# Optimization experiments

Measured on AMD Instinct MI355X. Metric: run time of the kernel, lower is better.

## Reference

```python
import jax, jax.numpy as jnp
import numpy as np

HEADS = 12
EMBED = 768
HEAD_DIM = EMBED // HEADS


def setup_inputs() -> dict:
    key = jax.random.key(0)
    kx, kw, kb = jax.random.split(key, 3)
    x = jax.random.normal(kx, (8, 1024, EMBED), dtype=jnp.float32)
    # nn.Linear(embed, 3*embed): weight (3E, E), bias (3E,)
    W_qkv = jax.random.normal(kw, (3 * EMBED, EMBED), dtype=jnp.float32) * (1.0 / np.sqrt(EMBED))
    b_qkv = jax.random.normal(kb, (3 * EMBED,), dtype=jnp.float32) * 0.01
    return {"x": x, "W_qkv": W_qkv, "b_qkv": b_qkv}


def reference(x, W_qkv, b_qkv):
    b, n, e = x.shape
    qkv = x @ W_qkv.T + b_qkv                       # (b, n, 3E)
    qkv = qkv.reshape(b, n, HEADS, 3 * HEAD_DIM)    # (b, n, h, 3d)
    q, k, v = jnp.split(qkv, 3, axis=-1)            # each (b, n, h, d)
    scores = jnp.einsum('bihd,bjhd->bijh', q, k) / np.sqrt(HEAD_DIM)
    attn = jax.nn.softmax(scores, axis=-2)          # softmax over keys j (dim=-2)
    out = jnp.einsum('bijh,bjhd->bihd', attn, v)
    return out.reshape(b, n, e)
```

## Files before the change

kernel.cpp:

```cpp
#include <hip/hip_runtime.h>
#include <hip/hip_bf16.h>
#include <cstdint>

#define BATCH 8
#define SEQ   1024
#define EMB   768
#define HEADS 12
#define HDIM  64
#define C3    2304
#define MROWS (BATCH*SEQ)
#define NKT   (EMB / 32)
#define MTILES (MROWS / 128)
#define NTILES (C3 / 128)
#define XPACK_BLOCKS (MTILES * NKT)
#define WPACK_BLOCKS (NTILES * NKT)

typedef __attribute__((ext_vector_type(8)))  short bf16x8;
typedef __attribute__((ext_vector_type(4)))  short bf16x4;
typedef __attribute__((ext_vector_type(4)))  float f32x4;
typedef __attribute__((ext_vector_type(16))) float f32x16;

static __device__ inline short f2bf(float f) {
    union { float f; uint32_t u; } v; v.f = f;
    uint32_t u = v.u + 0x7fff + ((v.u >> 16) & 1);
    return (short)(u >> 16);
}

static __device__ __forceinline__ void gload_lds16(const short* g, short* l) {
    __builtin_amdgcn_global_load_lds(
        (const __attribute__((address_space(1))) unsigned int*)g,
        (__attribute__((address_space(3))) unsigned int*)l, 16, 0, 0);
}

__global__ __launch_bounds__(256) void pack_bf16(const float* __restrict__ x,
                                                 short* __restrict__ xb2,
                                                 const float* __restrict__ W,
                                                 short* __restrict__ Wb2) {
    const float* in;
    short* out;
    int blk;
    if (blockIdx.x < XPACK_BLOCKS) {
        in = x; out = xb2; blk = blockIdx.x;
    } else {
        in = W; out = Wb2; blk = blockIdx.x - XPACK_BLOCKS;
    }
    const int mt = blk / NKT;
    const int kt = blk % NKT;
    short* obase = out + (size_t)blk * 4096;

    #pragma unroll
    for (int p = 0; p < 2; ++p) {
        int idx = p * 256 + threadIdx.x;
        int r = idx >> 2, s = idx & 3;
        const float* src = in + (size_t)(mt * 128 + r) * EMB + kt * 32 + s * 8;
        float4 v0 = ((const float4*)src)[0];
        float4 v1 = ((const float4*)src)[1];
        bf16x8 o = { f2bf(v0.x), f2bf(v0.y), f2bf(v0.z), f2bf(v0.w),
                     f2bf(v1.x), f2bf(v1.y), f2bf(v1.z), f2bf(v1.w) };
        int S = ((4 * r + s) ^ (r & 7));
        *(bf16x8*)(obase + S * 8) = o;
    }
}

__global__ __launch_bounds__(256) void qkv_gemm_mfma(const short* __restrict__ Apk,
                                                     const short* __restrict__ Bpk,
                                                     const float* __restrict__ bias,
                                                     short* __restrict__ qkvb) {
    __shared__ short As[2][4096];
    __shared__ short Bs[2][4096];

    const int g    = blockIdx.x;
    const int xcd  = g & 7;
    const int ring = g >> 3;
    const int by   = xcd * 8 + (ring & 7);
    const int bx   = ring >> 3;

    const int t    = threadIdx.x;
    const int w    = t >> 6;
    const int lane = t & 63;
    const int s4   = lane >> 4;
    const int r15  = lane & 15;
    const int m0 = by * 128, n0 = bx * 128;
    const int wm = (w & 1) * 64, wn = (w >> 1) * 64;

    const short* Ab = Apk + (size_t)by * (NKT * 4096);
    const short* Bb = Bpk + (size_t)bx * (NKT * 4096);

    int offA[4], offB[4];
    #pragma unroll
    for (int i = 0; i < 4; ++i) {
        int ra = wm + i * 16 + r15;
        offA[i] = ((4 * ra + s4) ^ (ra & 7)) << 3;
        int rb = wn + i * 16 + r15;
        offB[i] = ((4 * rb + s4) ^ (rb & 7)) << 3;
    }

    const int seg0 = w * 2;

#define STAGE(buf, kt) do {                                                   \
        const short* _a = Ab + (size_t)(kt) * 4096;                           \
        const short* _b = Bb + (size_t)(kt) * 4096;                           \
        gload_lds16(_a + (seg0    ) * 512 + lane * 8, &As[buf][(seg0    ) * 512]); \
        gload_lds16(_b + (seg0    ) * 512 + lane * 8, &Bs[buf][(seg0    ) * 512]); \
        gload_lds16(_a + (seg0 + 1) * 512 + lane * 8, &As[buf][(seg0 + 1) * 512]); \
        gload_lds16(_b + (seg0 + 1) * 512 + lane * 8, &Bs[buf][(seg0 + 1) * 512]); \
    } while (0)

    f32x4 acc[4][4] = {};

#define COMPUTE(buf) do {                                                     \
        bf16x8 af[4], bff[4];                                                 \
        _Pragma("unroll")                                                     \
        for (int i = 0; i < 4; ++i) {                                         \
            af[i]  = *(const bf16x8*)&As[buf][offA[i]];                       \
            bff[i] = *(const bf16x8*)&Bs[buf][offB[i]];                       \
        }                                                                     \
        _Pragma("unroll")                                                     \
        for (int mi = 0; mi < 4; ++mi)                                        \
            _Pragma("unroll")                                                 \
            for (int ni = 0; ni < 4; ++ni)                                    \
                acc[mi][ni] = __builtin_amdgcn_mfma_f32_16x16x32_bf16(        \
                    af[mi], bff[ni], acc[mi][ni], 0, 0, 0);                   \
    } while (0)

    STAGE(0, 0);
    __syncthreads();

    for (int kt = 0; kt < NKT; kt += 2) {
        STAGE(1, kt + 1);
        COMPUTE(0);
        __syncthreads();
        if (kt + 2 < NKT) STAGE(0, kt + 2);
        COMPUTE(1);
        __syncthreads();
    }
#undef STAGE
#undef COMPUTE

    float bsv[4], scl[4];
    #pragma unroll
    for (int ni = 0; ni < 4; ++ni) {
        int n = n0 + wn + ni * 16 + r15;
        bsv[ni] = bias[n];
        scl[ni] = ((n % 192) < 64) ? 0.125f : 1.0f;
    }
    #pragma unroll
    for (int mi = 0; mi < 4; ++mi)
        #pragma unroll
        for (int ni = 0; ni < 4; ++ni) {
            int n = n0 + wn + ni * 16 + r15;
            #pragma unroll
            for (int reg = 0; reg < 4; ++reg) {
                int m = m0 + wm + mi * 16 + s4 * 4 + reg;
                qkvb[(size_t)m * C3 + n] = f2bf((acc[mi][ni][reg] + bsv[ni]) * scl[ni]);
            }
        }
}

__global__ __launch_bounds__(256) void v_transpose(const short* __restrict__ qkvb,
                                                   short* __restrict__ vt) {
    __shared__ int Lt[64][65];

    const int bh = blockIdx.x;
    const int jt = blockIdx.y;
    const int b = bh / HEADS, h = bh % HEADS;
    const int t = threadIdx.x;
    const int j0 = jt * 64;
    const size_t base = (size_t)b * SEQ * C3 + (size_t)h * 192 + 128;

    #pragma unroll
    for (int p = 0; p < 2; ++p) {
        int idx = p * 256 + t;
        int j = idx >> 3, d0 = (idx & 7) * 8;
        bf16x8 v = *(const bf16x8*)(qkvb + base + (size_t)(j0 + j) * C3 + d0);
        #pragma unroll
        for (int u = 0; u < 8; ++u)
            Lt[d0 + u][j] = (int)(unsigned short)v[u];
    }
    __syncthreads();
    #pragma unroll
    for (int p = 0; p < 2; ++p) {
        int idx = p * 256 + t;
        int d = idx >> 3, c8 = (idx & 7) * 8;
        bf16x8 o;
        #pragma unroll
        for (int u = 0; u < 8; ++u)
            o[u] = (short)Lt[d][c8 + u];
        *(bf16x8*)(vt + ((size_t)bh * 64 + d) * SEQ + j0 + c8) = o;
    }
}

#define LDP 72

__global__ __launch_bounds__(256, 3) void attn_mfma(const short* __restrict__ qkvb,
                                                    const short* __restrict__ vt,
                                                    float* __restrict__ out) {
    __shared__ short Ks[64][LDP];
    __shared__ short Vt[64][LDP];
    __shared__ short Ps[128][LDP];

    const int g    = blockIdx.x;
    const int qt   = g / (BATCH * HEADS);
    const int bh   = g % (BATCH * HEADS);
    const int b    = bh / HEADS;
    const int h    = bh % HEADS;
    const int t    = threadIdx.x;
    const int w    = t >> 6;
    const int lane = t & 63;
    const int c    = lane & 15;
    const int q    = lane >> 4;
    const int i0   = qt * 128;

    const size_t base = (size_t)b * SEQ * C3 + (size_t)h * 192;
    const short* vtb = vt + (size_t)bh * 64 * SEQ;

    #pragma unroll
    for (int p = 0; p < 4; ++p) {
        int idx = p * 256 + t;
        int i = idx >> 3, d0 = (idx & 7) << 3;
        *(bf16x8*)&Ps[i][d0] =
            *(const bf16x8*)(qkvb + base + (size_t)(i0 + i) * C3 + d0);
    }
    __syncthreads();
    bf16x8 aq[2][2];
    #pragma unroll
    for (int s = 0; s < 2; ++s) {
        aq[s][0] = *(bf16x8*)&Ps[w * 32 + s * 16 + c][q * 8];
        aq[s][1] = *(bf16x8*)&Ps[w * 32 + s * 16 + c][32 + q * 8];
    }

    f32x4 o[2][4] = {};
    float l_acc[2] = {0.f, 0.f};

    for (int kt = 0; kt < 16; ++kt) {
        const int j0 = kt * 64;
        __syncthreads();
        #pragma unroll
        for (int p = 0; p < 2; ++p) {
            int idx = p * 256 + t;
            int j = idx >> 3, d0 = (idx & 7) << 3;
            *(bf16x8*)&Ks[j][d0] =
                *(const bf16x8*)(qkvb + base + 64 + (size_t)(j0 + j) * C3 + d0);
        }
        #pragma unroll
        for (int p = 0; p < 2; ++p) {
            int idx = p * 256 + t;
            int d = idx >> 3, j8 = (idx & 7) << 3;
            *(bf16x8*)&Vt[d][j8] =
                *(const bf16x8*)(vtb + (size_t)d * SEQ + j0 + j8);
        }
        __syncthreads();

        bf16x8 ka[4][2];
        #pragma unroll
        for (int mt = 0; mt < 4; ++mt) {
            ka[mt][0] = *(bf16x8*)&Ks[mt * 16 + c][q * 8];
            ka[mt][1] = *(bf16x8*)&Ks[mt * 16 + c][32 + q * 8];
        }

        f32x4 s[2][4];
        #pragma unroll
        for (int ss = 0; ss < 2; ++ss)
            #pragma unroll
            for (int mt = 0; mt < 4; ++mt) {
                f32x4 acc = {0.f, 0.f, 0.f, 0.f};
                acc = __builtin_amdgcn_mfma_f32_16x16x32_bf16(ka[mt][0], aq[ss][0], acc, 0, 0, 0);
                acc = __builtin_amdgcn_mfma_f32_16x16x32_bf16(ka[mt][1], aq[ss][1], acc, 0, 0, 0);
                s[ss][mt] = acc;
            }

        #pragma unroll
        for (int ss = 0; ss < 2; ++ss)
            #pragma unroll
            for (int mt = 0; mt < 4; ++mt) {
                float p0 = __expf(s[ss][mt][0]);
                float p1 = __expf(s[ss][mt][1]);
                float p2 = __expf(s[ss][mt][2]);
                float p3 = __expf(s[ss][mt][3]);
                l_acc[ss] += (p0 + p1) + (p2 + p3);
                bf16x4 pw = { f2bf(p0), f2bf(p1), f2bf(p2), f2bf(p3) };
                *(bf16x4*)&Ps[w * 32 + ss * 16 + c][mt * 16 + 4 * q] = pw;
            }

        bf16x8 vb[4][2];
        #pragma unroll
        for (int dt = 0; dt < 4; ++dt) {
            vb[dt][0] = *(bf16x8*)&Vt[dt * 16 + c][q * 8];
            vb[dt][1] = *(bf16x8*)&Vt[dt * 16 + c][32 + q * 8];
        }

        #pragma unroll
        for (int ss = 0; ss < 2; ++ss) {
            bf16x8 ap0 = *(bf16x8*)&Ps[w * 32 + ss * 16 + c][q * 8];
            bf16x8 ap1 = *(bf16x8*)&Ps[w * 32 + ss * 16 + c][32 + q * 8];
            #pragma unroll
            for (int dt = 0; dt < 4; ++dt) {
                o[ss][dt] = __builtin_amdgcn_mfma_f32_16x16x32_bf16(ap0, vb[dt][0], o[ss][dt], 0, 0, 0);
                o[ss][dt] = __builtin_amdgcn_mfma_f32_16x16x32_bf16(ap1, vb[dt][1], o[ss][dt], 0, 0, 0);
            }
        }
    }

    float linv[2][4];
    #pragma unroll
    for (int ss = 0; ss < 2; ++ss) {
        float v = l_acc[ss];
        v += __shfl_xor(v, 16, 64);
        v += __shfl_xor(v, 32, 64);
        #pragma unroll
        for (int r = 0; r < 4; ++r)
            linv[ss][r] = 1.0f / __shfl(v, 4 * q + r, 64);
    }

    #pragma unroll
    for (int ss = 0; ss < 2; ++ss)
        #pragma unroll
        for (int dt = 0; dt < 4; ++dt)
            #pragma unroll
            for (int r = 0; r < 4; ++r) {
                int i = w * 32 + ss * 16 + q * 4 + r;
                out[((size_t)b * SEQ + i0 + i) * EMB + h * HDIM + dt * 16 + c]
                    = o[ss][dt][r] * linv[ss][r];
            }
}

extern "C" void kernel_launch(void* const* d_in, const int* in_sizes, int n_in,
                              void* d_out, int out_size, void* d_ws, size_t ws_size,
                              hipStream_t stream) {
    const float* x    = (const float*)d_in[0];
    const float* W    = (const float*)d_in[1];
    const float* bias = (const float*)d_in[2];
    float* out = (float*)d_out;

    short* xb2  = (short*)d_ws;
    short* Wb2  = xb2 + (size_t)MROWS * EMB;
    short* qkvb = Wb2 + (size_t)C3 * EMB;
    short* vt   = qkvb + (size_t)MROWS * C3;

    pack_bf16<<<XPACK_BLOCKS + WPACK_BLOCKS, 256, 0, stream>>>(x, xb2, W, Wb2);

    qkv_gemm_mfma<<<1152, 256, 0, stream>>>(xb2, Wb2, bias, qkvb);

    dim3 g2(BATCH * HEADS, SEQ / 64);
    v_transpose<<<g2, 256, 0, stream>>>(qkvb, vt);

    attn_mfma<<<BATCH * HEADS * (SEQ / 128), 256, 0, stream>>>(qkvb, vt, out);
}
```

Baseline: 170.3 us.

## Load K and V fragments directly from global memory, dropping LDS staging

Removes the shared-memory tiles for K and V and the two block barriers per key tile. Each wave now loads its MFMA operand fragments straight from global memory. K for the next tile is prefetched into registers right after the score MFMAs, software-pipelining the loads, and Q is also loaded directly. Each of the four waves now issues its own redundant global/L2 reads of the same K/V tiles instead of sharing one LDS copy. Launch bounds drop from 3 to 2 blocks per SM to leave room for the extra registers.

```diff
diff --git a/kernel.cpp b/kernel.cpp
--- a/kernel.cpp
+++ b/kernel.cpp
@@ -192,11 +192,9 @@
 
 #define LDP 72
 
-__global__ __launch_bounds__(256, 3) void attn_mfma(const short* __restrict__ qkvb,
+__global__ __launch_bounds__(256, 2) void attn_mfma(const short* __restrict__ qkvb,
                                                     const short* __restrict__ vt,
                                                     float* __restrict__ out) {
-    __shared__ short Ks[64][LDP];
-    __shared__ short Vt[64][LDP];
     __shared__ short Ps[128][LDP];
 
     const int g    = blockIdx.x;
@@ -214,48 +212,42 @@
     const size_t base = (size_t)b * SEQ * C3 + (size_t)h * 192;
     const short* vtb = vt + (size_t)bh * 64 * SEQ;
 
-    #pragma unroll
-    for (int p = 0; p < 4; ++p) {
-        int idx = p * 256 + t;
-        int i = idx >> 3, d0 = (idx & 7) << 3;
-        *(bf16x8*)&Ps[i][d0] =
-            *(const bf16x8*)(qkvb + base + (size_t)(i0 + i) * C3 + d0);
-    }
-    __syncthreads();
     bf16x8 aq[2][2];
-    #pragma unroll
-    for (int s = 0; s < 2; ++s) {
-        aq[s][0] = *(bf16x8*)&Ps[w * 32 + s * 16 + c][q * 8];
-        aq[s][1] = *(bf16x8*)&Ps[w * 32 + s * 16 + c][32 + q * 8];
+    {
+        const short* pq = qkvb + base + (size_t)(i0 + w * 32 + c) * C3 + q * 8;
+        #pragma unroll
+        for (int s = 0; s < 2; ++s) {
+            aq[s][0] = *(const bf16x8*)(pq + (size_t)s * 16 * C3);
+            aq[s][1] = *(const bf16x8*)(pq + (size_t)s * 16 * C3 + 32);
+        }
+    }
+
+    const short* pk[4];
+    const short* pv[4];
+    #pragma unroll
+    for (int mt = 0; mt < 4; ++mt)
+        pk[mt] = qkvb + base + 64 + (size_t)(mt * 16 + c) * C3 + q * 8;
+    #pragma unroll
+    for (int dt = 0; dt < 4; ++dt)
+        pv[dt] = vtb + (size_t)(dt * 16 + c) * SEQ + q * 8;
+
+    bf16x8 ka[4][2];
+    #pragma unroll
+    for (int mt = 0; mt < 4; ++mt) {
+        ka[mt][0] = *(const bf16x8*)(pk[mt]);
+        ka[mt][1] = *(const bf16x8*)(pk[mt] + 32);
     }
 
     f32x4 o[2][4] = {};
     float l_acc[2] = {0.f, 0.f};
 
     for (int kt = 0; kt < 16; ++kt) {
-        const int j0 = kt * 64;
-        __syncthreads();
-        #pragma unroll
-        for (int p = 0; p < 2; ++p) {
-            int idx = p * 256 + t;
-            int j = idx >> 3, d0 = (idx & 7) << 3;
-            *(bf16x8*)&Ks[j][d0] =
-                *(const bf16x8*)(qkvb + base + 64 + (size_t)(j0 + j) * C3 + d0);
-        }
-        #pragma unroll
-        for (int p = 0; p < 2; ++p) {
-            int idx = p * 256 + t;
-            int d = idx >> 3, j8 = (idx & 7) << 3;
-            *(bf16x8*)&Vt[d][j8] =
-                *(const bf16x8*)(vtb + (size_t)d * SEQ + j0 + j8);
-        }
-        __syncthreads();
-
-        bf16x8 ka[4][2];
-        #pragma unroll
-        for (int mt = 0; mt < 4; ++mt) {
-            ka[mt][0] = *(bf16x8*)&Ks[mt * 16 + c][q * 8];
-            ka[mt][1] = *(bf16x8*)&Ks[mt * 16 + c][32 + q * 8];
+        bf16x8 vb[4][2];
+        #pragma unroll
+        for (int dt = 0; dt < 4; ++dt) {
+            vb[dt][0] = *(const bf16x8*)(pv[dt]);
+            vb[dt][1] = *(const bf16x8*)(pv[dt] + 32);
+            pv[dt] += 64;
         }
 
         f32x4 s[2][4];
@@ -268,6 +260,14 @@
                 acc = __builtin_amdgcn_mfma_f32_16x16x32_bf16(ka[mt][1], aq[ss][1], acc, 0, 0, 0);
                 s[ss][mt] = acc;
             }
+
+        const int adv = (kt < 15) ? 64 * C3 : 0;
+        #pragma unroll
+        for (int mt = 0; mt < 4; ++mt) {
+            pk[mt] += adv;
+            ka[mt][0] = *(const bf16x8*)(pk[mt]);
+            ka[mt][1] = *(const bf16x8*)(pk[mt] + 32);
+        }
 
         #pragma unroll
         for (int ss = 0; ss < 2; ++ss)
@@ -282,13 +282,6 @@
                 *(bf16x4*)&Ps[w * 32 + ss * 16 + c][mt * 16 + 4 * q] = pw;
             }
 
-        bf16x8 vb[4][2];
-        #pragma unroll
-        for (int dt = 0; dt < 4; ++dt) {
-            vb[dt][0] = *(bf16x8*)&Vt[dt * 16 + c][q * 8];
-            vb[dt][1] = *(bf16x8*)&Vt[dt * 16 + c][32 + q * 8];
-        }
-
         #pragma unroll
         for (int ss = 0; ss < 2; ++ss) {
             bf16x8 ap0 = *(bf16x8*)&Ps[w * 32 + ss * 16 + c][q * 8];
```

Measured after the change: 215.6 us. 1.27x slower.
